# Optimization experiments

Hardware: AMD Instinct MI355X
Metric: run time of the kernel (lower is better)

The kernel has to match this reference:

```python
import jax, jax.numpy as jnp
import numpy as np
import math

B, S, DM, H, DH = 2, 2048, 1024, 16, 64  # batch, seq, d_model, heads, head_dim


def setup_inputs() -> dict:
    key = jax.random.key(0)
    ks = jax.random.split(key, 4)
    scale = 0.02
    return {
        "hidden_states": jax.random.normal(ks[0], (B, S, DM), jnp.float32),
        "Wq": jax.random.normal(ks[1], (DM, DM), jnp.float32) * scale,
        "bq": jnp.zeros((DM,), jnp.float32),
        "Wk": jax.random.normal(ks[2], (DM, DM), jnp.float32) * scale,
        "bk": jnp.zeros((DM,), jnp.float32),
        "Wv": jax.random.normal(ks[3], (DM, DM), jnp.float32) * scale,
        "bv": jnp.zeros((DM,), jnp.float32),
    }


def reference(hidden_states, Wq, bq, Wk, bk, Wv, bv):
    b, s, _ = hidden_states.shape

    def proj(W, bias):
        # torch Linear: x @ W.T + b, then transpose_for_scores -> [B,H,S,Dh]
        x = hidden_states @ W.T + bias
        return x.reshape(b, s, H, DH).transpose(0, 2, 1, 3)

    query = proj(Wq, bq)
    key = proj(Wk, bk)
    value = proj(Wv, bv)

    # qk_matmul input calibration stats (abs-max over whole tensor)
    q_max = jax.lax.stop_gradient(jnp.max(jnp.abs(query)))
    kT_max = jax.lax.stop_gradient(jnp.max(jnp.abs(key)))  # transpose doesn't change abs-max

    attn_weights = jnp.einsum('bhqd,bhkd->bhqk', query, key)  # [B,H,S,S]
    qk_out_max = jax.lax.stop_gradient(jnp.max(jnp.abs(attn_weights)))

    attn_weights = attn_weights / math.sqrt(DH)
    attn_weights = jax.nn.softmax(attn_weights.astype(jnp.float32), axis=-1).astype(query.dtype)
    # eval mode: dropout p=0.0; head_mask is None

    # v_matmul input stats; note source also records attn_weights abs-max as 'v_matmul_out' (faithful)
    aw_max = jax.lax.stop_gradient(jnp.max(jnp.abs(attn_weights)))
    v_max = jax.lax.stop_gradient(jnp.max(jnp.abs(value)))
    v_out_max = aw_max  # source bug: re-reads attn_weights for v_matmul_out

    attn_output = jnp.einsum('bhqk,bhkd->bhqd', attn_weights, value)
    attn_output = attn_output.transpose(0, 2, 1, 3).reshape(b, s, H * DH)
    return attn_output, q_max, kT_max, qk_out_max, aw_max, v_max, v_out_max
```

## Files before the change

### kernel.cpp

```cpp
#include <hip/hip_runtime.h>
#include <hip/hip_bf16.h>
#include <stdint.h>

typedef __attribute__((ext_vector_type(8))) short short8;
typedef __attribute__((ext_vector_type(4))) short short4v;
typedef __attribute__((ext_vector_type(4))) float f32x4;

#define MFMA(a, b, c) __builtin_amdgcn_mfma_f32_16x16x32_bf16((a), (b), (c), 0, 0, 0)

#define C1 0.18033688011112042f
#define INV_C1 5.545177444479562f

static __device__ __forceinline__ unsigned int f2bf2(float x, float y) {
  union { __hip_bfloat162 h; unsigned int u; } c;
  c.h = __float22bfloat162_rn(make_float2(x, y));
  return c.u;
}

static __device__ __forceinline__ float exp2_fast(float x) {
  float r;
  asm("v_exp_f32 %0, %1" : "=v"(r) : "v"(x));
  return r;
}
static __device__ __forceinline__ unsigned int cvtpk(float lo, float hi) {
  unsigned int r;
  asm("v_cvt_pk_bf16_f32 %0, %1, %2" : "=v"(r) : "v"(lo), "v"(hi));
  return r;
}

static __device__ __forceinline__ void atomic_max_f32(float* addr, float v) {
  atomicMax((int*)addr, __float_as_int(v));
}

static __device__ __forceinline__ void gl_lds16(const void* g, void* l) {
  __builtin_amdgcn_global_load_lds(
      (const __attribute__((address_space(1))) void*)g,
      (__attribute__((address_space(3))) void*)l, 16, 0, 0);
}

__global__ __launch_bounds__(256) void k_cvt(
    const float* __restrict__ X, const float* __restrict__ Wq,
    const float* __restrict__ Wk, const float* __restrict__ Wv,
    short* __restrict__ Xb, short* __restrict__ Wb) {
  const int y = blockIdx.y;
  const int i = (blockIdx.x * 256 + threadIdx.x) * 8;
  const float* src;
  short* dstbase;
  if (y == 0) {
    if (i >= 4096 * 1024) return;
    src = X;
    dstbase = Xb;
  } else {
    if (i >= 1048576) return;
    src = (y == 1) ? Wq : (y == 2) ? Wk : Wv;
    dstbase = Wb + (y - 1) * 1048576;
  }
  const float4 a = *(const float4*)(src + i);
  const float4 b = *(const float4*)(src + i + 4);
  union { unsigned int u[4]; short8 s; } P;
  P.u[0] = f2bf2(a.x, a.y);
  P.u[1] = f2bf2(a.z, a.w);
  P.u[2] = f2bf2(b.x, b.y);
  P.u[3] = f2bf2(b.z, b.w);
  const int s = i >> 10, c0 = i & 1023;
  const int off = (((s >> 7) * 32 + (c0 >> 5)) * 4 + ((c0 >> 3) & 3)) * 1024 +
                  (s & 127) * 8;
  *(short8*)(dstbase + off) = P.s;
}

__global__ __launch_bounds__(256) void k_qkv(
    const short* __restrict__ Xb, const short* __restrict__ Wball,
    const float* __restrict__ bq, const float* __restrict__ bk,
    const float* __restrict__ bv,
    short* __restrict__ Qo, short* __restrict__ Ko, short* __restrict__ Vo,
    float* __restrict__ stats) {
  const int fid = (blockIdx.z * 32 + blockIdx.y) * 8 + blockIdx.x;
  const int sid = (fid & 7) * 96 + (fid >> 3);
  const int colb = sid & 7;
  const int zy = sid >> 3;
  const int z = zy >> 5;
  const int yb = zy & 31;

  const float* bias = (z == 0) ? bq : (z == 1) ? bk : bv;
  short* out = (z == 0) ? Qo : (z == 1) ? Ko : Vo;
  const bool qk = (z < 2);

  __shared__ __align__(16) short B0s[8192];
  __shared__ __align__(16) short B1s[8192];
  __shared__ __align__(16) short B2s[8192];
  __shared__ float red[4];

  const int t = threadIdx.x;
  const int lane = t & 63;
  const int w = t >> 6;
  const int l16 = lane & 15, quad = lane >> 4;
  const int wr = (w >> 1) * 64, wc = (w & 1) * 64;
  const int row0 = yb * 128;
  const int col0 = colb * 128;

  const short* ag = Xb + yb * 131072 + w * 512 + lane * 8;
  const short* bg = Wball + z * 1048576 + colb * 131072 + w * 512 + lane * 8;

  const int f0b = qk ? 4096 : 0, f0r = qk ? wc : wr;
  const int f1b = qk ? 0 : 4096, f1r = qk ? wr : wc;
  const int cq = quad * 1024;

  f32x4 acc[4][4];
#pragma unroll
  for (int i = 0; i < 4; ++i)
#pragma unroll
    for (int j = 0; j < 4; ++j) acc[i][j] = {0.f, 0.f, 0.f, 0.f};

#define STAGE(buf, ko_)                                  \
  do {                                                   \
    gl_lds16(ag + (ko_), (buf) + w * 512);               \
    gl_lds16(ag + (ko_) + 2048, (buf) + 2048 + w * 512); \
    gl_lds16(bg + (ko_), (buf) + 4096 + w * 512);        \
    gl_lds16(bg + (ko_) + 2048, (buf) + 6144 + w * 512); \
  } while (0)

#define COMPUTE(buf)                                                   \
  do {                                                                 \
    short8 fr0[4], fr1[4];                                             \
    _Pragma("unroll") for (int a = 0; a < 4; ++a)                      \
        fr0[a] = *(const short8*)&(buf)[f0b + cq + (f0r + a * 16 + l16) * 8]; \
    _Pragma("unroll") for (int b = 0; b < 4; ++b)                      \
        fr1[b] = *(const short8*)&(buf)[f1b + cq + (f1r + b * 16 + l16) * 8]; \
    _Pragma("unroll") for (int a = 0; a < 4; ++a)                      \
        _Pragma("unroll") for (int b = 0; b < 4; ++b)                  \
            acc[a][b] = MFMA(fr0[a], fr1[b], acc[a][b]);               \
  } while (0)

#define WAITBAR(n)                                                          \
  do {                                                                      \
    asm volatile("s_waitcnt lgkmcnt(0) vmcnt(" #n ")\n\ts_barrier" ::: "memory"); \
    __builtin_amdgcn_sched_barrier(0);                                      \
  } while (0)

  STAGE(B0s, 0);
  STAGE(B1s, 4096);
  WAITBAR(4);
  int ks = 8192;
#pragma unroll
  for (int i = 0; i < 10; ++i) {
    STAGE(B2s, ks); ks += 4096; COMPUTE(B0s); WAITBAR(4);
    STAGE(B0s, ks); ks += 4096; COMPUTE(B1s); WAITBAR(4);
    STAGE(B1s, ks); ks += 4096; COMPUTE(B2s); WAITBAR(4);
  }
  COMPUTE(B0s);
  WAITBAR(0);
  COMPUTE(B1s);
#undef STAGE
#undef COMPUTE
#undef WAITBAR

  const float qs = (z == 0) ? C1 : 1.0f;
  float amax = 0.f;
  if (qk) {
#pragma unroll
    for (int a = 0; a < 4; ++a) {
      const int dg = col0 + wc + a * 16 + quad * 4;
      const float4 b4 = *(const float4*)&bias[dg];
      const int h = dg >> 6, dl = dg & 63;
#pragma unroll
      for (int b = 0; b < 4; ++b) {
        const int sg = row0 + wr + b * 16 + l16;
        const float y0 = acc[a][b][0] + b4.x;
        const float y1 = acc[a][b][1] + b4.y;
        const float y2 = acc[a][b][2] + b4.z;
        const float y3 = acc[a][b][3] + b4.w;
        amax = fmaxf(amax, fmaxf(fmaxf(fabsf(y0), fabsf(y1)), fmaxf(fabsf(y2), fabsf(y3))));
        union { unsigned int u[2]; short4v s; } pk;
        pk.u[0] = cvtpk(y0 * qs, y1 * qs);
        pk.u[1] = cvtpk(y2 * qs, y3 * qs);
        const int bidx = sg >> 11, sl = sg & 2047;
        *(short4v*)&out[(size_t)(((bidx << 4) | h) * 2048 + sl) * 64 + dl] = pk.s;
      }
    }
  } else {
#pragma unroll
    for (int a = 0; a < 4; ++a) {
      const int sg = row0 + wr + a * 16 + quad * 4;
      const int bidx = sg >> 11, sl = sg & 2047;
#pragma unroll
      for (int b = 0; b < 4; ++b) {
        const int dg = col0 + wc + b * 16 + l16;
        const float bvf = bias[dg];
        const int h = dg >> 6, dl = dg & 63;
        const float y0 = acc[a][b][0] + bvf;
        const float y1 = acc[a][b][1] + bvf;
        const float y2 = acc[a][b][2] + bvf;
        const float y3 = acc[a][b][3] + bvf;
        amax = fmaxf(amax, fmaxf(fmaxf(fabsf(y0), fabsf(y1)), fmaxf(fabsf(y2), fabsf(y3))));
        union { unsigned int u[2]; short4v s; } pk;
        pk.u[0] = cvtpk(y0, y1);
        pk.u[1] = cvtpk(y2, y3);
        *(short4v*)&out[(size_t)(((bidx << 4) | h) * 64 + dl) * 2048 + sl] = pk.s;
      }
    }
  }
#pragma unroll
  for (int off = 32; off > 0; off >>= 1)
    amax = fmaxf(amax, __shfl_xor(amax, off, 64));
  if (lane == 0) red[w] = amax;
  __syncthreads();
  if (t == 0) {
    float m = fmaxf(fmaxf(red[0], red[1]), fmaxf(red[2], red[3]));
    atomic_max_f32(&stats[z], m);
  }
}

__global__ __launch_bounds__(512) void k_attn(
    const short* __restrict__ Q, const short* __restrict__ K,
    const short* __restrict__ V, float* __restrict__ O,
    float* __restrict__ stats) {
  const int fid = blockIdx.y * 16 + blockIdx.x;
  const int sid = ((fid & 7) << 6) + (fid >> 3);
  const int bh = sid >> 4;
  const int q0 = (sid & 15) << 7;
  const short* Qh = Q + (size_t)bh * 2048 * 64;
  const short* Kh = K + (size_t)bh * 2048 * 64;
  const short* Vh = V + (size_t)bh * 2048 * 64;

  __shared__ __align__(16) short Ks[64 * 64];
  __shared__ __align__(16) short Vts[64 * 64];
  __shared__ __align__(16) short Ps[8][16 * 64];
  __shared__ float redA[8], redB[8];

  const int t = threadIdx.x, lane = t & 63, w = t >> 6;
  const int l16 = lane & 15, quad = lane >> 4;
  const int srow = t >> 3;
  const int sslot = t & 7;
  const int wslot = (sslot ^ (srow & 7)) * 8;
  const int rsw = (l16 & 7);
  short* myPs = &Ps[w][0];

  short8 bq0, bq1;
  {
    const short* qsrc = Qh + (q0 + w * 16 + l16) * 64 + quad * 8;
    bq0 = *(const short8*)qsrc;
    bq1 = *(const short8*)(qsrc + 32);
  }

  float m_lane = -1e30f, l_lane = 0.f, xmin_lane = 1e30f;
  f32x4 o_acc[4];
#pragma unroll
  for (int jn = 0; jn < 4; ++jn) o_acc[jn] = {0.f, 0.f, 0.f, 0.f};
  const f32x4 zero = {0.f, 0.f, 0.f, 0.f};

  const int ksl0 = (quad ^ rsw) * 8;
  const int ksl1 = ((quad ^ rsw) ^ 4) * 8;

  short8 pk0 = *(const short8*)(Kh + srow * 64 + sslot * 8);
  short8 pv0 = *(const short8*)(Vh + srow * 2048 + sslot * 8);

  for (int kt = 0; kt < 32; ++kt) {
    __syncthreads();
    *(short8*)&Ks[srow * 64 + wslot] = pk0;
    *(short8*)&Vts[srow * 64 + wslot] = pv0;
    {
      const int ktn = (kt < 31) ? kt + 1 : 31;
      pk0 = *(const short8*)(Kh + (ktn * 64 + srow) * 64 + sslot * 8);
      pv0 = *(const short8*)(Vh + srow * 2048 + ktn * 64 + sslot * 8);
    }
    __syncthreads();

    f32x4 sacc[4];
#pragma unroll
    for (int j = 0; j < 4; ++j) {
      const int kb = (j * 16 + l16) * 64;
      short8 kf0 = *(const short8*)&Ks[kb + ksl0];
      short8 kf1 = *(const short8*)&Ks[kb + ksl1];
      sacc[j] = MFMA(kf1, bq1, MFMA(kf0, bq0, zero));
    }

    {
      float pmax = m_lane, psum = l_lane, xmn = xmin_lane;
#pragma unroll
      for (int j = 0; j < 4; ++j) {
        const float x0 = sacc[j][0], x1 = sacc[j][1];
        const float x2 = sacc[j][2], x3 = sacc[j][3];
        pmax = fmaxf(fmaxf(x0, fmaxf(x1, x2)), fmaxf(x3, pmax));
        xmn = fminf(fminf(x0, fminf(x1, x2)), fminf(x3, xmn));
        const float e0 = exp2_fast(x0), e1 = exp2_fast(x1);
        const float e2 = exp2_fast(x2), e3 = exp2_fast(x3);
        psum += (e0 + e1) + (e2 + e3);
        union { unsigned int u[2]; short4v s; } pk;
        pk.u[0] = cvtpk(e0, e1);
        pk.u[1] = cvtpk(e2, e3);
        *(short4v*)&myPs[l16 * 64 + ((j * 16 + quad * 4) ^ (rsw << 3))] = pk.s;
      }
      m_lane = pmax;
      l_lane = psum;
      xmin_lane = xmn;
    }
    asm volatile("" ::: "memory");

#pragma unroll
    for (int tstep = 0; tstep < 2; ++tstep) {
      const int psl = (tstep * 32 + quad * 8) ^ (rsw << 3);
      short8 ap = *(const short8*)&myPs[l16 * 64 + psl];
#pragma unroll
      for (int jn = 0; jn < 4; ++jn) {
        short8 vf = *(const short8*)&Vts[(jn * 16 + l16) * 64 + psl];
        o_acc[jn] = MFMA(ap, vf, o_acc[jn]);
      }
    }
    asm volatile("" ::: "memory");
  }

  float l = l_lane;
  l += __shfl_xor(l, 16, 64);
  l += __shfl_xor(l, 32, 64);
  float m = m_lane;
  m = fmaxf(m, __shfl_xor(m, 16, 64));
  m = fmaxf(m, __shfl_xor(m, 32, 64));
  float xm = xmin_lane;
  xm = fminf(xm, __shfl_xor(xm, 16, 64));
  xm = fminf(xm, __shfl_xor(xm, 32, 64));
  float aw = exp2_fast(m) / l;
  float qkx = fmaxf(m, -xm);

  const int bidx = bh >> 4, h = bh & 15;
  float linv[4];
#pragma unroll
  for (int r = 0; r < 4; ++r)
    linv[r] = 1.0f / __shfl(l, quad * 4 + r, 16);
#pragma unroll
  for (int jn = 0; jn < 4; ++jn) {
    const int d = jn * 16 + l16;
#pragma unroll
    for (int r = 0; r < 4; ++r) {
      const int s_row = q0 + w * 16 + quad * 4 + r;
      O[((size_t)(bidx * 2048 + s_row) * 1024) + h * 64 + d] =
          o_acc[jn][r] * linv[r];
    }
  }

#pragma unroll
  for (int off = 32; off > 0; off >>= 1) {
    qkx = fmaxf(qkx, __shfl_xor(qkx, off, 64));
    aw = fmaxf(aw, __shfl_xor(aw, off, 64));
  }
  if (lane == 0) {
    redA[w] = qkx;
    redB[w] = aw;
  }
  __syncthreads();
  if (t == 0) {
    float a = redA[0], b = redB[0];
#pragma unroll
    for (int i = 1; i < 8; ++i) {
      a = fmaxf(a, redA[i]);
      b = fmaxf(b, redB[i]);
    }
    atomic_max_f32(&stats[3], a * INV_C1);
    atomic_max_f32(&stats[4], b);
  }
}

__global__ void k_fin(const float* __restrict__ stats, float* __restrict__ out) {
  const int i = threadIdx.x;
  if (i == 0) out[0] = stats[0];
  if (i == 1) out[1] = stats[1];
  if (i == 2) out[2] = stats[3];
  if (i == 3) out[3] = stats[4];
  if (i == 4) out[4] = stats[2];
  if (i == 5) out[5] = stats[4];
}

extern "C" void kernel_launch(void* const* d_in, const int* in_sizes, int n_in,
                              void* d_out, int out_size, void* d_ws, size_t ws_size,
                              hipStream_t stream) {
  const float* X = (const float*)d_in[0];
  const float* Wq = (const float*)d_in[1];
  const float* bq = (const float*)d_in[2];
  const float* Wk = (const float*)d_in[3];
  const float* bk = (const float*)d_in[4];
  const float* Wv = (const float*)d_in[5];
  const float* bv = (const float*)d_in[6];
  float* out = (float*)d_out;

  float* stats = (float*)d_ws;
  short* base = (short*)((char*)d_ws + 4096);
  short* Qb = base;
  short* Kb = base + 4194304;
  short* Vb = base + 8388608;
  short* Xb = base + 12582912;
  short* Wb = base + 16777216;

  k_cvt<<<dim3(2048, 4), 256, 0, stream>>>(X, Wq, Wk, Wv, Xb, Wb);
  k_qkv<<<dim3(8, 32, 3), 256, 0, stream>>>(Xb, Wb, bq, bk, bv, Qb, Kb, Vb, stats);
  k_attn<<<dim3(16, 32), 512, 0, stream>>>(Qb, Kb, Vb, out, stats);
  k_fin<<<1, 64, 0, stream>>>(stats, out + 4194304);
}
```

Before: 181.1 us.

## Pre-swizzle K/V tiles in projection output and triple-buffer attention loads via direct-to-LDS

The projection kernel now writes K and V in a tiled, pre-swizzled 64x64 block layout that matches the attention kernel's LDS layout, with V stored transposed per tile. This lets the attention kernel copy each tile contiguously from global memory straight into LDS (gl_lds16) through a three-stage ring buffer with a single waitcnt+barrier per step. It replaces the register-staged loads and the two barriers per iteration. It also raises wave priority around the MFMA sections. The cost is triple the K/V LDS footprint (about 48KB more), which may limit occupancy.

```diff
diff --git a/kernel.cpp b/kernel.cpp
--- a/kernel.cpp
+++ b/kernel.cpp
@@ -154,9 +154,8 @@
 #undef COMPUTE
 #undef WAITBAR
 
-  const float qs = (z == 0) ? C1 : 1.0f;
   float amax = 0.f;
-  if (qk) {
+  if (z == 0) {
 #pragma unroll
     for (int a = 0; a < 4; ++a) {
       const int dg = col0 + wc + a * 16 + quad * 4;
@@ -171,10 +170,33 @@
         const float y3 = acc[a][b][3] + b4.w;
         amax = fmaxf(amax, fmaxf(fmaxf(fabsf(y0), fabsf(y1)), fmaxf(fabsf(y2), fabsf(y3))));
         union { unsigned int u[2]; short4v s; } pk;
-        pk.u[0] = cvtpk(y0 * qs, y1 * qs);
-        pk.u[1] = cvtpk(y2 * qs, y3 * qs);
+        pk.u[0] = cvtpk(y0 * C1, y1 * C1);
+        pk.u[1] = cvtpk(y2 * C1, y3 * C1);
         const int bidx = sg >> 11, sl = sg & 2047;
-        *(short4v*)&out[(size_t)(((bidx << 4) | h) * 2048 + sl) * 64 + dl] = pk.s;
+        *(short4v*)&out[(size_t)((((bidx << 4) | h) * 2048 + sl)) * 64 + dl] = pk.s;
+      }
+    }
+  } else if (z == 1) {
+#pragma unroll
+    for (int a = 0; a < 4; ++a) {
+      const int dg = col0 + wc + a * 16 + quad * 4;
+      const float4 b4 = *(const float4*)&bias[dg];
+      const int h = dg >> 6, dl = dg & 63;
+#pragma unroll
+      for (int b = 0; b < 4; ++b) {
+        const int sg = row0 + wr + b * 16 + l16;
+        const float y0 = acc[a][b][0] + b4.x;
+        const float y1 = acc[a][b][1] + b4.y;
+        const float y2 = acc[a][b][2] + b4.z;
+        const float y3 = acc[a][b][3] + b4.w;
+        amax = fmaxf(amax, fmaxf(fmaxf(fabsf(y0), fabsf(y1)), fmaxf(fabsf(y2), fabsf(y3))));
+        union { unsigned int u[2]; short4v s; } pk;
+        pk.u[0] = cvtpk(y0, y1);
+        pk.u[1] = cvtpk(y2, y3);
+        const int bidx = sg >> 11, sl = sg & 2047;
+        const int ktt = sl >> 6, row = sl & 63;
+        const size_t tb = ((size_t)(((bidx << 4) | h) * 32 + ktt) * 64 + row) * 64;
+        *(short4v*)&out[tb + (((dl >> 3) ^ (row & 7)) * 8) + (dl & 7)] = pk.s;
       }
     }
   } else {
@@ -182,6 +204,7 @@
     for (int a = 0; a < 4; ++a) {
       const int sg = row0 + wr + a * 16 + quad * 4;
       const int bidx = sg >> 11, sl = sg & 2047;
+      const int ktt = sl >> 6, key = sl & 63;
 #pragma unroll
       for (int b = 0; b < 4; ++b) {
         const int dg = col0 + wc + b * 16 + l16;
@@ -195,7 +218,8 @@
         union { unsigned int u[2]; short4v s; } pk;
         pk.u[0] = cvtpk(y0, y1);
         pk.u[1] = cvtpk(y2, y3);
-        *(short4v*)&out[(size_t)(((bidx << 4) | h) * 64 + dl) * 2048 + sl] = pk.s;
+        const size_t tb = ((size_t)(((bidx << 4) | h) * 32 + ktt) * 64 + dl) * 64;
+        *(short4v*)&out[tb + (((key >> 3) ^ (dl & 7)) * 8) + (key & 7)] = pk.s;
       }
     }
   }
@@ -219,21 +243,19 @@
   const int bh = sid >> 4;
   const int q0 = (sid & 15) << 7;
   const short* Qh = Q + (size_t)bh * 2048 * 64;
-  const short* Kh = K + (size_t)bh * 2048 * 64;
-  const short* Vh = V + (size_t)bh * 2048 * 64;
-
-  __shared__ __align__(16) short Ks[64 * 64];
-  __shared__ __align__(16) short Vts[64 * 64];
+
+  __shared__ __align__(16) short Ks[3 * 4096];
+  __shared__ __align__(16) short Vts[3 * 4096];
   __shared__ __align__(16) short Ps[8][16 * 64];
   __shared__ float redA[8], redB[8];
 
   const int t = threadIdx.x, lane = t & 63, w = t >> 6;
   const int l16 = lane & 15, quad = lane >> 4;
-  const int srow = t >> 3;
-  const int sslot = t & 7;
-  const int wslot = (sslot ^ (srow & 7)) * 8;
   const int rsw = (l16 & 7);
   short* myPs = &Ps[w][0];
+
+  const short* kg = K + (size_t)bh * 131072 + w * 512 + lane * 8;
+  const short* vg = V + (size_t)bh * 131072 + w * 512 + lane * 8;
 
   short8 bq0, bq1;
   {
@@ -251,63 +273,77 @@
   const int ksl0 = (quad ^ rsw) * 8;
   const int ksl1 = ((quad ^ rsw) ^ 4) * 8;
 
-  short8 pk0 = *(const short8*)(Kh + srow * 64 + sslot * 8);
-  short8 pv0 = *(const short8*)(Vh + srow * 2048 + sslot * 8);
-
-  for (int kt = 0; kt < 32; ++kt) {
-    __syncthreads();
-    *(short8*)&Ks[srow * 64 + wslot] = pk0;
-    *(short8*)&Vts[srow * 64 + wslot] = pv0;
-    {
-      const int ktn = (kt < 31) ? kt + 1 : 31;
-      pk0 = *(const short8*)(Kh + (ktn * 64 + srow) * 64 + sslot * 8);
-      pv0 = *(const short8*)(Vh + srow * 2048 + ktn * 64 + sslot * 8);
-    }
-    __syncthreads();
-
-    f32x4 sacc[4];
-#pragma unroll
-    for (int j = 0; j < 4; ++j) {
-      const int kb = (j * 16 + l16) * 64;
-      short8 kf0 = *(const short8*)&Ks[kb + ksl0];
-      short8 kf1 = *(const short8*)&Ks[kb + ksl1];
-      sacc[j] = MFMA(kf1, bq1, MFMA(kf0, bq0, zero));
-    }
-
-    {
-      float pmax = m_lane, psum = l_lane, xmn = xmin_lane;
-#pragma unroll
-      for (int j = 0; j < 4; ++j) {
-        const float x0 = sacc[j][0], x1 = sacc[j][1];
-        const float x2 = sacc[j][2], x3 = sacc[j][3];
-        pmax = fmaxf(fmaxf(x0, fmaxf(x1, x2)), fmaxf(x3, pmax));
-        xmn = fminf(fminf(x0, fminf(x1, x2)), fminf(x3, xmn));
-        const float e0 = exp2_fast(x0), e1 = exp2_fast(x1);
-        const float e2 = exp2_fast(x2), e3 = exp2_fast(x3);
-        psum += (e0 + e1) + (e2 + e3);
-        union { unsigned int u[2]; short4v s; } pk;
-        pk.u[0] = cvtpk(e0, e1);
-        pk.u[1] = cvtpk(e2, e3);
-        *(short4v*)&myPs[l16 * 64 + ((j * 16 + quad * 4) ^ (rsw << 3))] = pk.s;
-      }
-      m_lane = pmax;
-      l_lane = psum;
-      xmin_lane = xmn;
-    }
-    asm volatile("" ::: "memory");
-
-#pragma unroll
-    for (int tstep = 0; tstep < 2; ++tstep) {
-      const int psl = (tstep * 32 + quad * 8) ^ (rsw << 3);
-      short8 ap = *(const short8*)&myPs[l16 * 64 + psl];
-#pragma unroll
-      for (int jn = 0; jn < 4; ++jn) {
-        short8 vf = *(const short8*)&Vts[(jn * 16 + l16) * 64 + psl];
-        o_acc[jn] = MFMA(ap, vf, o_acc[jn]);
-      }
-    }
-    asm volatile("" ::: "memory");
-  }
+#define ASTAGE(cb, ko_)                            \
+  do {                                             \
+    gl_lds16(kg + (ko_), Ks + (cb) * 4096 + w * 512);  \
+    gl_lds16(vg + (ko_), Vts + (cb) * 4096 + w * 512); \
+  } while (0)
+
+#define AWAITBAR(n)                                                         \
+  do {                                                                      \
+    asm volatile("s_waitcnt lgkmcnt(0) vmcnt(" #n ")\n\ts_barrier" ::: "memory"); \
+    __builtin_amdgcn_sched_barrier(0);                                      \
+  } while (0)
+
+#define ACOMPUTE(cb)                                                        \
+  do {                                                                      \
+    const int kbase = (cb) * 4096;                                          \
+    f32x4 sacc[4];                                                          \
+    __builtin_amdgcn_s_setprio(1);                                          \
+    _Pragma("unroll") for (int j = 0; j < 4; ++j) {                         \
+      const int kb = kbase + (j * 16 + l16) * 64;                           \
+      short8 kf0 = *(const short8*)&Ks[kb + ksl0];                          \
+      short8 kf1 = *(const short8*)&Ks[kb + ksl1];                          \
+      sacc[j] = MFMA(kf1, bq1, MFMA(kf0, bq0, zero));                       \
+    }                                                                       \
+    __builtin_amdgcn_s_setprio(0);                                          \
+    {                                                                       \
+      float pmax = m_lane, psum = l_lane, xmn = xmin_lane;                  \
+      _Pragma("unroll") for (int j = 0; j < 4; ++j) {                       \
+        const float x0 = sacc[j][0], x1 = sacc[j][1];                       \
+        const float x2 = sacc[j][2], x3 = sacc[j][3];                       \
+        pmax = fmaxf(fmaxf(x0, fmaxf(x1, x2)), fmaxf(x3, pmax));            \
+        xmn = fminf(fminf(x0, fminf(x1, x2)), fminf(x3, xmn));              \
+        const float e0 = exp2_fast(x0), e1 = exp2_fast(x1);                 \
+        const float e2 = exp2_fast(x2), e3 = exp2_fast(x3);                 \
+        psum += (e0 + e1) + (e2 + e3);                                      \
+        union { unsigned int u[2]; short4v s; } pk;                         \
+        pk.u[0] = cvtpk(e0, e1);                                            \
+        pk.u[1] = cvtpk(e2, e3);                                            \
+        *(short4v*)&myPs[l16 * 64 + ((j * 16 + quad * 4) ^ (rsw << 3))] = pk.s; \
+      }                                                                     \
+      m_lane = pmax; l_lane = psum; xmin_lane = xmn;                        \
+    }                                                                       \
+    asm volatile("" ::: "memory");                                          \
+    __builtin_amdgcn_s_setprio(1);                                          \
+    _Pragma("unroll") for (int tstep = 0; tstep < 2; ++tstep) {             \
+      const int psl = (tstep * 32 + quad * 8) ^ (rsw << 3);                 \
+      short8 ap = *(const short8*)&myPs[l16 * 64 + psl];                    \
+      _Pragma("unroll") for (int jn = 0; jn < 4; ++jn) {                    \
+        short8 vf = *(const short8*)&Vts[kbase + (jn * 16 + l16) * 64 + psl]; \
+        o_acc[jn] = MFMA(ap, vf, o_acc[jn]);                                \
+      }                                                                     \
+    }                                                                       \
+    __builtin_amdgcn_s_setprio(0);                                          \
+    asm volatile("" ::: "memory");                                          \
+  } while (0)
+
+  ASTAGE(0, 0);
+  ASTAGE(1, 4096);
+  AWAITBAR(2);
+  int ko = 8192;
+#pragma unroll
+  for (int i = 0; i < 10; ++i) {
+    ASTAGE(2, ko); ko += 4096; ACOMPUTE(0); AWAITBAR(2);
+    ASTAGE(0, ko); ko += 4096; ACOMPUTE(1); AWAITBAR(2);
+    ASTAGE(1, ko); ko += 4096; ACOMPUTE(2); AWAITBAR(2);
+  }
+  ACOMPUTE(0);
+  AWAITBAR(0);
+  ACOMPUTE(1);
+#undef ASTAGE
+#undef AWAITBAR
+#undef ACOMPUTE
 
   float l = l_lane;
   l += __shfl_xor(l, 16, 64);
```

After: 177.4 us. -2.1%, faster.
